# Kernel optimization log

Measured on AMD Instinct MI355X. Metric: run time of the kernel, lower is better.

The kernel has to match this reference:

```python
import jax, jax.numpy as jnp
import numpy as np

N_NODES = 65536
N_PER = 1024      # nodes per graph
NUM_GRAPHS = 64
N_EDGES = 1048576
IN_DIM = 192
PE_DIM = 64
HIDDEN = 256
LATENT = 128
POOL_RATIO = 0.5
K_PER = int(np.ceil(POOL_RATIO * N_PER))  # 512 kept per graph


def setup_inputs() -> dict:
    key = jax.random.key(0)
    ks = jax.random.split(key, 12)
    x_raw = jax.random.normal(ks[0], (N_NODES, IN_DIM), dtype=jnp.float32)
    sincos_pe = jax.random.normal(ks[1], (N_NODES, PE_DIM), dtype=jnp.float32)
    edge_index = jax.random.randint(ks[2], (2, N_EDGES), 0, N_NODES, dtype=jnp.int64)
    batch = (jnp.arange(N_NODES, dtype=jnp.int64) // N_PER)
    eps = jax.random.normal(ks[3], (N_NODES, LATENT), dtype=jnp.float32)
    # learned parameters (GCNConv: Linear no-bias weight + separate bias; TopKPooling weight)
    def glorot(k, shape):
        lim = float(np.sqrt(6.0 / (shape[0] + shape[1])))
        return jax.random.uniform(k, shape, jnp.float32, -lim, lim)
    W1 = glorot(ks[4], (IN_DIM + PE_DIM, HIDDEN))
    b1 = jnp.zeros((HIDDEN,), jnp.float32)
    Wmu = glorot(ks[5], (HIDDEN, LATENT))
    bmu = jnp.zeros((LATENT,), jnp.float32)
    Wlv = glorot(ks[6], (HIDDEN, LATENT))
    blv = jnp.zeros((LATENT,), jnp.float32)
    w_pool = jax.random.uniform(ks[7], (LATENT,), jnp.float32, -1.0, 1.0) / np.sqrt(LATENT)
    return {"x_raw": x_raw, "sincos_pe": sincos_pe, "edge_index": edge_index,
            "batch": batch, "eps": eps, "W1": W1, "b1": b1, "Wmu": Wmu,
            "bmu": bmu, "Wlv": Wlv, "blv": blv, "w_pool": w_pool}


def _gcn_conv(x, W, b, src, dst, n):
    # PyG GCNConv: x' = D^{-1/2}(A+I)D^{-1/2} (x W) + b, self-loops already in src/dst
    h = x @ W                                   # [N, out]
    deg = jnp.zeros((n,), h.dtype).at[dst].add(1.0)
    dinv = jax.lax.rsqrt(deg)                   # deg >= 1 thanks to self-loops
    norm = dinv[src] * dinv[dst]                # [E+N]
    msg = norm[:, None] * h[src]                # gather (irregular)
    return jax.ops.segment_sum(msg, dst, num_segments=n) + b


def reference(x_raw, sincos_pe, edge_index, batch, eps, W1, b1, Wmu, bmu, Wlv, blv, w_pool):
    n = x_raw.shape[0]
    loops = jnp.arange(n, dtype=edge_index.dtype)
    src = jnp.concatenate([edge_index[0], loops])
    dst = jnp.concatenate([edge_index[1], loops])

    x_in = jnp.concatenate([x_raw, sincos_pe], axis=-1)
    h = jax.nn.relu(_gcn_conv(x_in, W1, b1, src, dst, n))
    mu = _gcn_conv(h, Wmu, bmu, src, dst, n)
    logvar = _gcn_conv(h, Wlv, blv, src, dst, n)
    z = mu + eps * jnp.exp(0.5 * logvar)

    # TopKPooling: score = tanh((z . w)/||w||); keep top ratio per graph
    score = jnp.tanh((z @ w_pool) / jnp.linalg.norm(w_pool))   # [N]
    s2 = score.reshape(NUM_GRAPHS, N_PER)
    _, idx = jax.lax.top_k(s2, K_PER)                           # descending per graph
    perm = (idx + (jnp.arange(NUM_GRAPHS) * N_PER)[:, None]).reshape(-1)
    z_pool = z[perm] * score[perm][:, None]
    mu_pool = mu[perm]
    logvar_pool = logvar[perm]
    batch_pool = batch[perm]
    return z_pool, mu_pool, logvar_pool, batch_pool, perm
```

## Files before the change

### kernel.cpp

```cpp
#include <hip/hip_runtime.h>
#include <hip/hip_fp16.h>
#include <math.h>

#define NN      65536
#define NE      1048576
#define NPER    1024
#define NGRAPH  64
#define KPER    512
#define IND     192
#define PED     64
#define HID     256
#define LAT     128

#define OFF_CNT     0u
#define OFF_ROWPTR  65536u
#define OFF_CUR     132096u
#define OFF_DINV    198656u
#define OFF_EPK     264192u
#define OFF_INVWN   2361344u
#define OFF_KEEP    2361360u
#define OFF_SCORE   2395136u
#define OFF_WT1     2460672u
#define OFF_WT2     2493440u
#define OFF_T0B     2526208u
#define OFF_HB      6720512u
#define OFF_MUB     6720512u
#define OFF_LVB     10914816u

#define OUT_MU      4194304
#define OUT_LV      8388608
#define OUT_BATCH   12582912
#define OUT_PERM    12615680

typedef __attribute__((ext_vector_type(8))) short short8;
typedef __attribute__((ext_vector_type(4))) float floatx4;

__device__ __forceinline__ unsigned short f2bf(float f) {
    unsigned int u = __float_as_uint(f);
    u += 0x7FFFu + ((u >> 16) & 1u);
    return (unsigned short)(u >> 16);
}
__device__ __forceinline__ float bf2f(unsigned short u) {
    return __uint_as_float(((unsigned int)u) << 16);
}
__device__ __forceinline__ unsigned int pack2bf(float x, float y) {
    const unsigned int ux = __float_as_uint(x) + 0x8000u;
    const unsigned int uy = __float_as_uint(y) + 0x8000u;
    return __builtin_amdgcn_perm(uy, ux, 0x07060302u);
}
__device__ __forceinline__ unsigned char f2e5(float f) {
    unsigned short u = __half_as_ushort(__float2half(f));
    u += (unsigned short)(0x7Fu + ((u >> 8) & 1u));
    return (unsigned char)(u >> 8);
}
__device__ __forceinline__ unsigned int pack4e5(float v0, float v1, float v2, float v3) {
#if __has_builtin(__builtin_amdgcn_cvt_pk_bf8_f32)
    const int t0 = __builtin_amdgcn_cvt_pk_bf8_f32(v0, v1, 0, false);
    return (unsigned int)__builtin_amdgcn_cvt_pk_bf8_f32(v2, v3, t0, true);
#else
    return (unsigned int)f2e5(v0) | ((unsigned int)f2e5(v1) << 8) |
           ((unsigned int)f2e5(v2) << 16) | ((unsigned int)f2e5(v3) << 24);
#endif
}
__device__ __forceinline__ __half2 e5lo(unsigned int u) {
    return __builtin_bit_cast(__half2, __builtin_amdgcn_perm(u, 0u, 0x05000400u));
}
__device__ __forceinline__ __half2 e5hi(unsigned int u) {
    return __builtin_bit_cast(__half2, __builtin_amdgcn_perm(u, 0u, 0x07000600u));
}

__global__ __launch_bounds__(256) void k_count(const int* __restrict__ ei, int* __restrict__ cnt) {
    const int g = blockIdx.x * 256 + threadIdx.x;
    const int4 d4 = *(const int4*)(ei + NE + g * 4);
    atomicAdd(&cnt[d4.x], 1);
    atomicAdd(&cnt[d4.y], 1);
    atomicAdd(&cnt[d4.z], 1);
    atomicAdd(&cnt[d4.w], 1);
}

__global__ __launch_bounds__(256) void k_scanA(const int* __restrict__ cnt, int* __restrict__ rp,
                                               float* __restrict__ dinv, int* __restrict__ bsum) {
    __shared__ int sh[256];
    const int t = threadIdx.x, b = blockIdx.x;
    const int i = b * 256 + t;
    const int c = cnt[i];
    sh[t] = c;
    __syncthreads();
    for (int d = 1; d < 256; d <<= 1) {
        const int v = (t >= d) ? sh[t - d] : 0;
        __syncthreads();
        sh[t] += v;
        __syncthreads();
    }
    rp[i] = sh[t] - c;
    dinv[i] = 1.0f / sqrtf((float)(c + 1));
    if (t == 255) bsum[b] = sh[t];
}

__global__ __launch_bounds__(256) void k_scanB(int* __restrict__ bsum) {
    __shared__ int sh[256];
    const int t = threadIdx.x;
    const int c = bsum[t];
    sh[t] = c;
    __syncthreads();
    for (int d = 1; d < 256; d <<= 1) {
        const int v = (t >= d) ? sh[t - d] : 0;
        __syncthreads();
        sh[t] += v;
        __syncthreads();
    }
    bsum[t] = sh[t] - c;
}

__global__ __launch_bounds__(256) void k_scanC(int* __restrict__ rp, const int* __restrict__ bsum) {
    const int t = threadIdx.x, b = blockIdx.x;
    const int i = b * 256 + t;
    rp[i] += bsum[b];
    if (i == NN - 1) rp[NN] = NE;
}

__global__ __launch_bounds__(256) void k_scatter(const int* __restrict__ ei, const int* __restrict__ rp,
                                                 int* __restrict__ cur, const float* __restrict__ dinv,
                                                 int2* __restrict__ epk) {
    int e = blockIdx.x * 256 + threadIdx.x;
    int s = ei[e];
    int d = ei[NE + e];
    int pos = rp[d] + atomicAdd(&cur[d], 1);
    epk[pos] = make_int2(s, __float_as_int(dinv[s] * dinv[d]));
}

__global__ __launch_bounds__(128) void k_wnorm(const float* __restrict__ wp, float* __restrict__ invwn) {
    __shared__ float red[128];
    int t = threadIdx.x;
    float v = wp[t];
    red[t] = v * v;
    __syncthreads();
    for (int s = 64; s > 0; s >>= 1) {
        if (t < s) red[t] += red[t + s];
        __syncthreads();
    }
    if (t == 0) invwn[0] = 1.0f / sqrtf(red[0]);
}

__global__ __launch_bounds__(256) void k_prepw(const float* __restrict__ W1, const float* __restrict__ Wmu,
                                               const float* __restrict__ Wlv, unsigned short* __restrict__ wt1,
                                               unsigned short* __restrict__ wt2) {
    const int n = blockIdx.x, k = threadIdx.x;
    wt1[n * 256 + k] = f2bf(W1[k * 256 + n]);
    wt2[n * 256 + k] = f2bf((n < 128) ? Wmu[k * 128 + n] : Wlv[k * 128 + (n - 128)]);
}

template <int MODE>
__global__ __launch_bounds__(256, 2) void k_gemm(const float* __restrict__ A0f, const float* __restrict__ A1f,
                                                 const unsigned short* __restrict__ Ah,
                                                 const unsigned short* __restrict__ Wt,
                                                 unsigned char* __restrict__ Cb) {
    __shared__ unsigned short lds[2][12288];
    const int tid = threadIdx.x;
    const int w = __builtin_amdgcn_readfirstlane(tid >> 6);
    const int lane = tid & 63;
    const int l = lane & 15, q = lane >> 4;
    const int Rbase = blockIdx.x * 128;
    const int mtb = (w >> 1) * 4;
    const int ntb = (w & 1) * 8;

    const int rs = tid >> 1;
    const int ch = tid & 1;
    const int stile = rs >> 4, sl = rs & 15, q0 = ch * 2;
    const int uA = (stile * 4 + q0) * 16 + sl;

    floatx4 acc[8][4];
#pragma unroll
    for (int j = 0; j < 8; ++j)
#pragma unroll
        for (int m = 0; m < 4; ++m) acc[j][m] = (floatx4)0.0f;

    auto stage = [&](int ks, int buf) {
        if (MODE == 0) {
            const float* p; int ld, col;
            const int k = ks * 32 + ch * 16;
            if (ks < 6) { p = A0f; ld = IND; col = k; }
            else        { p = A1f; ld = PED; col = k - IND; }
            const float* src = p + (size_t)(Rbase + rs) * ld + col;
            unsigned int pk[8];
#pragma unroll
            for (int j = 0; j < 16; j += 4) {
                const float4 t = *(const float4*)(src + j);
                pk[j / 2]     = pack2bf(t.x, t.y);
                pk[j / 2 + 1] = pack2bf(t.z, t.w);
            }
            *(uint4*)&lds[buf][uA * 8]        = *(uint4*)&pk[0];
            *(uint4*)&lds[buf][(uA + 16) * 8] = *(uint4*)&pk[4];
        } else {
            const unsigned short* src = Ah + (size_t)(Rbase + rs) * 256 + ks * 32 + ch * 16;
            *(uint4*)&lds[buf][uA * 8]        = ((const uint4*)src)[0];
            *(uint4*)&lds[buf][(uA + 16) * 8] = ((const uint4*)src)[1];
        }
#pragma unroll
        for (int rep = 0; rep < 2; ++rep) {
            const int n = rep * 128 + rs;
            const unsigned short* srcB = Wt + (size_t)n * 256 + ks * 32 + ch * 16;
            const uint4 w0 = ((const uint4*)srcB)[0];
            const uint4 w1 = ((const uint4*)srcB)[1];
            const int uB = ((n >> 4) * 4 + q0) * 16 + (n & 15);
            *(uint4*)&lds[buf][4096 + uB * 8]        = w0;
            *(uint4*)&lds[buf][4096 + (uB + 16) * 8] = w1;
        }
    };

    stage(0, 0);
    __syncthreads();
#pragma unroll
    for (int ks = 0; ks < 8; ++ks) {
        const int cur = ks & 1;
        if (ks < 7) stage(ks + 1, cur ^ 1);
        short8 a[4];
#pragma unroll
        for (int m = 0; m < 4; ++m)
            a[m] = *(const short8*)&lds[cur][(((mtb + m) * 4 + q) * 16 + l) * 8];
#pragma unroll
        for (int j = 0; j < 8; ++j) {
            const short8 b = *(const short8*)&lds[cur][4096 + (((ntb + j) * 4 + q) * 16 + l) * 8];
#pragma unroll
            for (int m = 0; m < 4; ++m)
                acc[j][m] = __builtin_amdgcn_mfma_f32_16x16x32_bf16(b, a[m], acc[j][m], 0, 0, 0);
        }
        if (ks < 7) __syncthreads();
    }

#pragma unroll
    for (int m = 0; m < 4; ++m) {
        unsigned char* rbase = Cb + (size_t)(Rbase + (mtb + m) * 16 + l) * 256 + q * 4;
#pragma unroll
        for (int j = 0; j < 8; ++j) {
            const floatx4 v = acc[j][m];
            *(unsigned int*)(rbase + (ntb + j) * 16) = pack4e5(v[0], v[1], v[2], v[3]);
        }
    }
}

template <int PHASE>
__global__ __launch_bounds__(256) void k_agg(const unsigned char* __restrict__ tb, const int* __restrict__ rp,
                                             const int2* __restrict__ epk, const float* __restrict__ dinv,
                                             const float* __restrict__ bias0, const float* __restrict__ bias1,
                                             const float* __restrict__ eps, const float* __restrict__ wp,
                                             const float* __restrict__ invwn, unsigned short* __restrict__ hb,
                                             unsigned short* __restrict__ mub, unsigned short* __restrict__ lvb,
                                             float* __restrict__ score) {
    const int wv = __builtin_amdgcn_readfirstlane(threadIdx.x >> 6);
    const int lane = threadIdx.x & 63;
    const int node = blockIdx.x * 4 + wv;
    const int c0 = lane * 4;
    const float di = dinv[node];
    const unsigned char* tbc = tb + c0;

    const unsigned int vs = *(const unsigned int*)(tbc + ((size_t)node << 8));
    const __half2 ws2 = __float2half2_rn(di * di);
    __half2 a01 = __hmul2(ws2, e5lo(vs));
    __half2 a23 = __hmul2(ws2, e5hi(vs));
    __half2 b01 = __float2half2_rn(0.0f);
    __half2 b23 = __float2half2_rn(0.0f);

    const int lane8 = lane & 7;
    const int beg = rp[node], end = rp[node + 1];
    int p = beg;
    if (p + 8 <= end) {
        int2 emv = epk[p + lane8];
        int2 env = epk[p + 8 + lane8];
        unsigned int v[8];
#pragma unroll
        for (int i = 0; i < 8; ++i)
            v[i] = *(const unsigned int*)(tbc + ((size_t)__builtin_amdgcn_readlane(emv.x, i) << 8));
        while (p + 16 <= end) {
            const int2 efv = epk[p + 16 + lane8];
            unsigned int u[8];
#pragma unroll
            for (int i = 0; i < 8; ++i)
                u[i] = *(const unsigned int*)(tbc + ((size_t)__builtin_amdgcn_readlane(env.x, i) << 8));
#pragma unroll
            for (int i = 0; i < 8; i += 2) {
                const __half2 wA = __float2half2_rn(__int_as_float(__builtin_amdgcn_readlane(emv.y, i)));
                const __half2 wB = __float2half2_rn(__int_as_float(__builtin_amdgcn_readlane(emv.y, i + 1)));
                a01 = __hfma2(wA, e5lo(v[i]), a01);     a23 = __hfma2(wA, e5hi(v[i]), a23);
                b01 = __hfma2(wB, e5lo(v[i + 1]), b01); b23 = __hfma2(wB, e5hi(v[i + 1]), b23);
            }
            emv = env; env = efv;
#pragma unroll
            for (int i = 0; i < 8; ++i) v[i] = u[i];
            p += 8;
        }
#pragma unroll
        for (int i = 0; i < 8; i += 2) {
            const __half2 wA = __float2half2_rn(__int_as_float(__builtin_amdgcn_readlane(emv.y, i)));
            const __half2 wB = __float2half2_rn(__int_as_float(__builtin_amdgcn_readlane(emv.y, i + 1)));
            a01 = __hfma2(wA, e5lo(v[i]), a01);     a23 = __hfma2(wA, e5hi(v[i]), a23);
            b01 = __hfma2(wB, e5lo(v[i + 1]), b01); b23 = __hfma2(wB, e5hi(v[i + 1]), b23);
        }
        p += 8;
    }
    if (p + 4 <= end) {
        const int2 e0 = epk[p], e1 = epk[p + 1], e2 = epk[p + 2], e3 = epk[p + 3];
        const unsigned int v0 = *(const unsigned int*)(tbc + ((size_t)__builtin_amdgcn_readfirstlane(e0.x) << 8));
        const unsigned int v1 = *(const unsigned int*)(tbc + ((size_t)__builtin_amdgcn_readfirstlane(e1.x) << 8));
        const unsigned int v2 = *(const unsigned int*)(tbc + ((size_t)__builtin_amdgcn_readfirstlane(e2.x) << 8));
        const unsigned int v3 = *(const unsigned int*)(tbc + ((size_t)__builtin_amdgcn_readfirstlane(e3.x) << 8));
        const __half2 w0 = __float2half2_rn(__int_as_float(e0.y));
        const __half2 w1 = __float2half2_rn(__int_as_float(e1.y));
        const __half2 w2 = __float2half2_rn(__int_as_float(e2.y));
        const __half2 w3 = __float2half2_rn(__int_as_float(e3.y));
        a01 = __hfma2(w0, e5lo(v0), a01); a23 = __hfma2(w0, e5hi(v0), a23);
        b01 = __hfma2(w1, e5lo(v1), b01); b23 = __hfma2(w1, e5hi(v1), b23);
        a01 = __hfma2(w2, e5lo(v2), a01); a23 = __hfma2(w2, e5hi(v2), a23);
        b01 = __hfma2(w3, e5lo(v3), b01); b23 = __hfma2(w3, e5hi(v3), b23);
        p += 4;
    }
    for (; p < end; ++p) {
        const int2 e = epk[p];
        const unsigned int v = *(const unsigned int*)(tbc + ((size_t)__builtin_amdgcn_readfirstlane(e.x) << 8));
        const __half2 w2 = __float2half2_rn(__int_as_float(e.y));
        a01 = __hfma2(w2, e5lo(v), a01);
        a23 = __hfma2(w2, e5hi(v), a23);
    }
    a01 = __hadd2(a01, b01);
    a23 = __hadd2(a23, b23);
    const float2 flo = __half22float2(a01);
    const float2 fhi = __half22float2(a23);
    float4 acc = make_float4(flo.x, flo.y, fhi.x, fhi.y);

    if (PHASE == 0) {
        const float4 bb = *(const float4*)(bias0 + c0);
        ushort4 r;
        r.x = f2bf(fmaxf(acc.x + bb.x, 0.0f));
        r.y = f2bf(fmaxf(acc.y + bb.y, 0.0f));
        r.z = f2bf(fmaxf(acc.z + bb.z, 0.0f));
        r.w = f2bf(fmaxf(acc.w + bb.w, 0.0f));
        *(ushort4*)(hb + ((size_t)node << 8) + c0) = r;
    } else {
        const int cb = (lane & 31) * 4;
        const float* bias = (lane < 32) ? bias0 : bias1;
        const float4 bb = *(const float4*)(bias + cb);
        acc.x += bb.x; acc.y += bb.y; acc.z += bb.z; acc.w += bb.w;
        unsigned short* dst = (lane < 32) ? mub : lvb;
        ushort4 st;
        st.x = f2bf(acc.x); st.y = f2bf(acc.y); st.z = f2bf(acc.z); st.w = f2bf(acc.w);
        *(ushort4*)(dst + (size_t)node * 128 + cb) = st;
        float4 l4;
        l4.x = __shfl(acc.x, lane | 32, 64);
        l4.y = __shfl(acc.y, lane | 32, 64);
        l4.z = __shfl(acc.z, lane | 32, 64);
        l4.w = __shfl(acc.w, lane | 32, 64);
        float partial = 0.0f;
        if (lane < 32) {
            const float4 e4 = *(const float4*)(eps + (size_t)node * 128 + cb);
            const float4 w4 = *(const float4*)(wp + cb);
            float zx = fmaf(e4.x, expf(0.5f * l4.x), acc.x);
            float zy = fmaf(e4.y, expf(0.5f * l4.y), acc.y);
            float zz = fmaf(e4.z, expf(0.5f * l4.z), acc.z);
            float zw = fmaf(e4.w, expf(0.5f * l4.w), acc.w);
            partial = zx * w4.x + zy * w4.y + zz * w4.z + zw * w4.w;
        }
        for (int off = 16; off > 0; off >>= 1) partial += __shfl_xor(partial, off, 64);
        if (lane == 0) score[node] = tanhf(partial * invwn[0]);
    }
}

__global__ __launch_bounds__(512) void k_topk(const float* __restrict__ score, const int* __restrict__ batch,
                                              int* __restrict__ keep, float* __restrict__ out) {
    __shared__ float sk[1024];
    __shared__ int si[1024];
    const int g = blockIdx.x, t = threadIdx.x;
    for (int i = t; i < 1024; i += 512) {
        sk[i] = score[g * 1024 + i];
        si[i] = i;
    }
    __syncthreads();
    for (int k = 2; k <= 1024; k <<= 1) {
        for (int j = k >> 1; j > 0; j >>= 1) {
            for (int base = 0; base < 1024; base += 512) {
                int i = base + t;
                int ixj = i ^ j;
                if (ixj > i) {
                    float a = sk[i], b = sk[ixj];
                    int ia = si[i], ib = si[ixj];
                    bool before = (a > b) || (a == b && ia < ib);
                    bool up = ((i & k) == 0);
                    bool sw = up ? (!before) : before;
                    if (sw) {
                        sk[i] = b; si[i] = ib;
                        sk[ixj] = a; si[ixj] = ia;
                    }
                }
            }
            __syncthreads();
        }
    }
    if (t < KPER) {
        int node = g * 1024 + si[t];
        keep[g * KPER + t] = node;
        out[OUT_BATCH + g * KPER + t] = (float)batch[node];
        out[OUT_PERM + g * KPER + t] = (float)node;
    }
}

__global__ __launch_bounds__(128) void k_gather(const int* __restrict__ keep,
                                                const unsigned short* __restrict__ mub,
                                                const unsigned short* __restrict__ lvb,
                                                const float* __restrict__ eps,
                                                const float* __restrict__ score, float* __restrict__ out) {
    const int kidx = blockIdx.x;
    const int c = threadIdx.x;
    const int node = keep[kidx];
    const float m = bf2f(mub[(size_t)node * 128 + c]);
    const float l = bf2f(lvb[(size_t)node * 128 + c]);
    const float e = eps[(size_t)node * 128 + c];
    const float z = fmaf(e, expf(0.5f * l), m);
    const float s = score[node];
    out[(size_t)kidx * 128 + c] = z * s;
    out[OUT_MU + (size_t)kidx * 128 + c] = m;
    out[OUT_LV + (size_t)kidx * 128 + c] = l;
}

extern "C" void kernel_launch(void* const* d_in, const int* in_sizes, int n_in,
                              void* d_out, int out_size, void* d_ws, size_t ws_size,
                              hipStream_t stream) {
    (void)in_sizes; (void)n_in; (void)out_size; (void)ws_size;
    const float* x_raw = (const float*)d_in[0];
    const float* pe    = (const float*)d_in[1];
    const int*   ei    = (const int*)d_in[2];
    const int*   batch = (const int*)d_in[3];
    const float* eps   = (const float*)d_in[4];
    const float* W1    = (const float*)d_in[5];
    const float* b1    = (const float*)d_in[6];
    const float* Wmu   = (const float*)d_in[7];
    const float* bmu   = (const float*)d_in[8];
    const float* Wlv   = (const float*)d_in[9];
    const float* blv   = (const float*)d_in[10];
    const float* wp    = (const float*)d_in[11];
    float* ws = (float*)d_ws;
    int*  iws = (int*)d_ws;
    int2* epk = (int2*)(iws + OFF_EPK);
    unsigned short* wt1  = (unsigned short*)(ws + OFF_WT1);
    unsigned short* wt2  = (unsigned short*)(ws + OFF_WT2);
    unsigned char*  t0b  = (unsigned char*)(ws + OFF_T0B);
    unsigned short* hb16 = (unsigned short*)(ws + OFF_HB);
    unsigned short* mub  = (unsigned short*)(ws + OFF_MUB);
    unsigned short* lvb  = (unsigned short*)(ws + OFF_LVB);
    float* out = (float*)d_out;

    hipMemsetAsync(iws + OFF_CNT, 0, 65536 * 4, stream);
    hipMemsetAsync(iws + OFF_CUR, 0, 65536 * 4, stream);

    k_count<<<NE / 1024, 256, 0, stream>>>(ei, iws + OFF_CNT);
    k_scanA<<<256, 256, 0, stream>>>(iws + OFF_CNT, iws + OFF_ROWPTR, ws + OFF_DINV, iws + OFF_KEEP);
    k_scanB<<<1, 256, 0, stream>>>(iws + OFF_KEEP);
    k_scanC<<<256, 256, 0, stream>>>(iws + OFF_ROWPTR, iws + OFF_KEEP);
    k_scatter<<<NE / 256, 256, 0, stream>>>(ei, iws + OFF_ROWPTR, iws + OFF_CUR, ws + OFF_DINV, epk);
    k_wnorm<<<1, 128, 0, stream>>>(wp, ws + OFF_INVWN);
    k_prepw<<<256, 256, 0, stream>>>(W1, Wmu, Wlv, wt1, wt2);

    k_gemm<0><<<NN / 128, 256, 0, stream>>>(x_raw, pe, nullptr, wt1, t0b);
    k_agg<0><<<NN / 4, 256, 0, stream>>>(t0b, iws + OFF_ROWPTR, epk, ws + OFF_DINV,
                                         b1, nullptr, nullptr, nullptr, nullptr,
                                         hb16, nullptr, nullptr, nullptr);
    k_gemm<1><<<NN / 128, 256, 0, stream>>>(nullptr, nullptr, hb16, wt2, t0b);
    k_agg<1><<<NN / 4, 256, 0, stream>>>(t0b, iws + OFF_ROWPTR, epk, ws + OFF_DINV,
                                         bmu, blv, eps, wp, ws + OFF_INVWN,
                                         nullptr, mub, lvb, ws + OFF_SCORE);
    k_topk<<<NGRAPH, 512, 0, stream>>>(ws + OFF_SCORE, batch, iws + OFF_KEEP, out);
    k_gather<<<NGRAPH * KPER, 128, 0, stream>>>(iws + OFF_KEEP, mub, lvb, eps,
                                                ws + OFF_SCORE, out);
}
```

Baseline: 422.3 us.

## Slice fp8 feature table by column, pack edge metadata, atomically accumulate score

The GEMM output is stored column-sliced (32-byte slices per node), so each aggregation wave handles 8 nodes by 32 columns and gathers hit a smaller, cache-friendlier slice. Edge records are packed into 32 bits (16-bit source index plus fp16 weight), halving the edge stream. The score is now built from partial sums via atomicAdd across slices, with tanh moved into the gather kernel. Because per-lane work now runs serially over each node's edges with a per-lane data-dependent loop, wave divergence and the extra atomics may cost time. The 16-bit source index is enough only because there are 65536 nodes.

```diff
diff --git a/kernel.cpp b/kernel.cpp
--- a/kernel.cpp
+++ b/kernel.cpp
@@ -68,6 +68,9 @@
 __device__ __forceinline__ __half2 e5hi(unsigned int u) {
     return __builtin_bit_cast(__half2, __builtin_amdgcn_perm(u, 0u, 0x07000600u));
 }
+__device__ __forceinline__ __half2 meta2w(unsigned int m) {
+    return __builtin_bit_cast(__half2, __builtin_amdgcn_perm(m, m, 0x07060706u));
+}
 
 __global__ __launch_bounds__(256) void k_count(const int* __restrict__ ei, int* __restrict__ cnt) {
     const int g = blockIdx.x * 256 + threadIdx.x;
@@ -121,12 +124,13 @@
 
 __global__ __launch_bounds__(256) void k_scatter(const int* __restrict__ ei, const int* __restrict__ rp,
                                                  int* __restrict__ cur, const float* __restrict__ dinv,
-                                                 int2* __restrict__ epk) {
+                                                 unsigned int* __restrict__ epk) {
     int e = blockIdx.x * 256 + threadIdx.x;
     int s = ei[e];
     int d = ei[NE + e];
     int pos = rp[d] + atomicAdd(&cur[d], 1);
-    epk[pos] = make_int2(s, __float_as_int(dinv[s] * dinv[d]));
+    const unsigned short hn = __half_as_ushort(__float2half(dinv[s] * dinv[d]));
+    epk[pos] = ((unsigned int)hn << 16) | (unsigned int)s;
 }
 
 __global__ __launch_bounds__(128) void k_wnorm(const float* __restrict__ wp, float* __restrict__ invwn) {
@@ -230,137 +234,99 @@
 
 #pragma unroll
     for (int m = 0; m < 4; ++m) {
-        unsigned char* rbase = Cb + (size_t)(Rbase + (mtb + m) * 16 + l) * 256 + q * 4;
+        const int row = Rbase + (mtb + m) * 16 + l;
 #pragma unroll
         for (int j = 0; j < 8; ++j) {
+            const int col = (ntb + j) * 16 + q * 4;
             const floatx4 v = acc[j][m];
-            *(unsigned int*)(rbase + (ntb + j) * 16) = pack4e5(v[0], v[1], v[2], v[3]);
+            *(unsigned int*)(Cb + ((size_t)(col >> 5) * NN + row) * 32 + (col & 31)) =
+                pack4e5(v[0], v[1], v[2], v[3]);
         }
     }
 }
 
 template <int PHASE>
 __global__ __launch_bounds__(256) void k_agg(const unsigned char* __restrict__ tb, const int* __restrict__ rp,
-                                             const int2* __restrict__ epk, const float* __restrict__ dinv,
+                                             const unsigned int* __restrict__ epk, const float* __restrict__ dinv,
                                              const float* __restrict__ bias0, const float* __restrict__ bias1,
                                              const float* __restrict__ eps, const float* __restrict__ wp,
-                                             const float* __restrict__ invwn, unsigned short* __restrict__ hb,
-                                             unsigned short* __restrict__ mub, unsigned short* __restrict__ lvb,
-                                             float* __restrict__ score) {
-    const int wv = __builtin_amdgcn_readfirstlane(threadIdx.x >> 6);
+                                             unsigned short* __restrict__ hb, unsigned short* __restrict__ mub,
+                                             unsigned short* __restrict__ lvb, float* __restrict__ score) {
     const int lane = threadIdx.x & 63;
-    const int node = blockIdx.x * 4 + wv;
-    const int c0 = lane * 4;
+    const int slice = blockIdx.x & 7;
+    const int node = (blockIdx.x >> 3) * 32 + (threadIdx.x >> 6) * 8 + (lane >> 3);
+    const int lo4 = (lane & 7) * 4;
+    const unsigned char* tsl = tb + ((size_t)slice * NN) * 32 + lo4;
+
     const float di = dinv[node];
-    const unsigned char* tbc = tb + c0;
-
-    const unsigned int vs = *(const unsigned int*)(tbc + ((size_t)node << 8));
+    const unsigned int vs = *(const unsigned int*)(tsl + ((size_t)node << 5));
     const __half2 ws2 = __float2half2_rn(di * di);
     __half2 a01 = __hmul2(ws2, e5lo(vs));
     __half2 a23 = __hmul2(ws2, e5hi(vs));
     __half2 b01 = __float2half2_rn(0.0f);
     __half2 b23 = __float2half2_rn(0.0f);
 
-    const int lane8 = lane & 7;
-    const int beg = rp[node], end = rp[node + 1];
-    int p = beg;
-    if (p + 8 <= end) {
-        int2 emv = epk[p + lane8];
-        int2 env = epk[p + 8 + lane8];
-        unsigned int v[8];
-#pragma unroll
-        for (int i = 0; i < 8; ++i)
-            v[i] = *(const unsigned int*)(tbc + ((size_t)__builtin_amdgcn_readlane(emv.x, i) << 8));
-        while (p + 16 <= end) {
-            const int2 efv = epk[p + 16 + lane8];
-            unsigned int u[8];
-#pragma unroll
-            for (int i = 0; i < 8; ++i)
-                u[i] = *(const unsigned int*)(tbc + ((size_t)__builtin_amdgcn_readlane(env.x, i) << 8));
-#pragma unroll
-            for (int i = 0; i < 8; i += 2) {
-                const __half2 wA = __float2half2_rn(__int_as_float(__builtin_amdgcn_readlane(emv.y, i)));
-                const __half2 wB = __float2half2_rn(__int_as_float(__builtin_amdgcn_readlane(emv.y, i + 1)));
-                a01 = __hfma2(wA, e5lo(v[i]), a01);     a23 = __hfma2(wA, e5hi(v[i]), a23);
-                b01 = __hfma2(wB, e5lo(v[i + 1]), b01); b23 = __hfma2(wB, e5hi(v[i + 1]), b23);
-            }
-            emv = env; env = efv;
-#pragma unroll
-            for (int i = 0; i < 8; ++i) v[i] = u[i];
-            p += 8;
-        }
-#pragma unroll
-        for (int i = 0; i < 8; i += 2) {
-            const __half2 wA = __float2half2_rn(__int_as_float(__builtin_amdgcn_readlane(emv.y, i)));
-            const __half2 wB = __float2half2_rn(__int_as_float(__builtin_amdgcn_readlane(emv.y, i + 1)));
-            a01 = __hfma2(wA, e5lo(v[i]), a01);     a23 = __hfma2(wA, e5hi(v[i]), a23);
-            b01 = __hfma2(wB, e5lo(v[i + 1]), b01); b23 = __hfma2(wB, e5hi(v[i + 1]), b23);
-        }
-        p += 8;
-    }
-    if (p + 4 <= end) {
-        const int2 e0 = epk[p], e1 = epk[p + 1], e2 = epk[p + 2], e3 = epk[p + 3];
-        const unsigned int v0 = *(const unsigned int*)(tbc + ((size_t)__builtin_amdgcn_readfirstlane(e0.x) << 8));
-        const unsigned int v1 = *(const unsigned int*)(tbc + ((size_t)__builtin_amdgcn_readfirstlane(e1.x) << 8));
-        const unsigned int v2 = *(const unsigned int*)(tbc + ((size_t)__builtin_amdgcn_readfirstlane(e2.x) << 8));
-        const unsigned int v3 = *(const unsigned int*)(tbc + ((size_t)__builtin_amdgcn_readfirstlane(e3.x) << 8));
-        const __half2 w0 = __float2half2_rn(__int_as_float(e0.y));
-        const __half2 w1 = __float2half2_rn(__int_as_float(e1.y));
-        const __half2 w2 = __float2half2_rn(__int_as_float(e2.y));
-        const __half2 w3 = __float2half2_rn(__int_as_float(e3.y));
+    int p = rp[node];
+    const int end = rp[node + 1];
+    unsigned int m0 = epk[p], m1 = epk[p + 1];
+    unsigned int v0 = *(const unsigned int*)(tsl + ((size_t)(m0 & 0xFFFFu) << 5));
+    unsigned int v1 = *(const unsigned int*)(tsl + ((size_t)(m1 & 0xFFFFu) << 5));
+    while (p + 2 <= end) {
+        const unsigned int n0 = epk[p + 2], n1 = epk[p + 3];
+        const unsigned int u0 = *(const unsigned int*)(tsl + ((size_t)(n0 & 0xFFFFu) << 5));
+        const unsigned int u1 = *(const unsigned int*)(tsl + ((size_t)(n1 & 0xFFFFu) << 5));
+        const __half2 w0 = meta2w(m0);
+        const __half2 w1 = meta2w(m1);
         a01 = __hfma2(w0, e5lo(v0), a01); a23 = __hfma2(w0, e5hi(v0), a23);
         b01 = __hfma2(w1, e5lo(v1), b01); b23 = __hfma2(w1, e5hi(v1), b23);
-        a01 = __hfma2(w2, e5lo(v2), a01); a23 = __hfma2(w2, e5hi(v2), a23);
-        b01 = __hfma2(w3, e5lo(v3), b01); b23 = __hfma2(w3, e5hi(v3), b23);
-        p += 4;
-    }
-    for (; p < end; ++p) {
-        const int2 e = epk[p];
-        const unsigned int v = *(const unsigned int*)(tbc + ((size_t)__builtin_amdgcn_readfirstlane(e.x) << 8));
-        const __half2 w2 = __float2half2_rn(__int_as_float(e.y));
-        a01 = __hfma2(w2, e5lo(v), a01);
-        a23 = __hfma2(w2, e5hi(v), a23);
+        m0 = n0; m1 = n1; v0 = u0; v1 = u1; p += 2;
+    }
+    if (p < end) {
+        const __half2 w0 = meta2w(m0);
+        a01 = __hfma2(w0, e5lo(v0), a01);
+        a23 = __hfma2(w0, e5hi(v0), a23);
     }
     a01 = __hadd2(a01, b01);
     a23 = __hadd2(a23, b23);
     const float2 flo = __half22float2(a01);
     const float2 fhi = __half22float2(a23);
     float4 acc = make_float4(flo.x, flo.y, fhi.x, fhi.y);
+    const int c = slice * 32 + lo4;
 
     if (PHASE == 0) {
-        const float4 bb = *(const float4*)(bias0 + c0);
+        const float4 bb = *(const float4*)(bias0 + c);
         ushort4 r;
         r.x = f2bf(fmaxf(acc.x + bb.x, 0.0f));
         r.y = f2bf(fmaxf(acc.y + bb.y, 0.0f));
         r.z = f2bf(fmaxf(acc.z + bb.z, 0.0f));
         r.w = f2bf(fmaxf(acc.w + bb.w, 0.0f));
-        *(ushort4*)(hb + ((size_t)node << 8) + c0) = r;
+        *(ushort4*)(hb + (size_t)node * 256 + c) = r;
     } else {
-        const int cb = (lane & 31) * 4;
-        const float* bias = (lane < 32) ? bias0 : bias1;
-        const float4 bb = *(const float4*)(bias + cb);
-        acc.x += bb.x; acc.y += bb.y; acc.z += bb.z; acc.w += bb.w;
-        unsigned short* dst = (lane < 32) ? mub : lvb;
-        ushort4 st;
-        st.x = f2bf(acc.x); st.y = f2bf(acc.y); st.z = f2bf(acc.z); st.w = f2bf(acc.w);
-        *(ushort4*)(dst + (size_t)node * 128 + cb) = st;
-        float4 l4;
-        l4.x = __shfl(acc.x, lane | 32, 64);
-        l4.y = __shfl(acc.y, lane | 32, 64);
-        l4.z = __shfl(acc.z, lane | 32, 64);
-        l4.w = __shfl(acc.w, lane | 32, 64);
-        float partial = 0.0f;
-        if (lane < 32) {
-            const float4 e4 = *(const float4*)(eps + (size_t)node * 128 + cb);
-            const float4 w4 = *(const float4*)(wp + cb);
-            float zx = fmaf(e4.x, expf(0.5f * l4.x), acc.x);
-            float zy = fmaf(e4.y, expf(0.5f * l4.y), acc.y);
-            float zz = fmaf(e4.z, expf(0.5f * l4.z), acc.z);
-            float zw = fmaf(e4.w, expf(0.5f * l4.w), acc.w);
-            partial = zx * w4.x + zy * w4.y + zz * w4.z + zw * w4.w;
-        }
-        for (int off = 16; off > 0; off >>= 1) partial += __shfl_xor(partial, off, 64);
-        if (lane == 0) score[node] = tanhf(partial * invwn[0]);
+        float partial;
+        if (c < 128) {
+            const float4 bb = *(const float4*)(bias0 + c);
+            acc.x += bb.x; acc.y += bb.y; acc.z += bb.z; acc.w += bb.w;
+            ushort4 st;
+            st.x = f2bf(acc.x); st.y = f2bf(acc.y); st.z = f2bf(acc.z); st.w = f2bf(acc.w);
+            *(ushort4*)(mub + (size_t)node * 128 + c) = st;
+            const float4 w4 = *(const float4*)(wp + c);
+            partial = acc.x * w4.x + acc.y * w4.y + acc.z * w4.z + acc.w * w4.w;
+        } else {
+            const int cl = c - 128;
+            const float4 bb = *(const float4*)(bias1 + cl);
+            acc.x += bb.x; acc.y += bb.y; acc.z += bb.z; acc.w += bb.w;
+            ushort4 st;
+            st.x = f2bf(acc.x); st.y = f2bf(acc.y); st.z = f2bf(acc.z); st.w = f2bf(acc.w);
+            *(ushort4*)(lvb + (size_t)node * 128 + cl) = st;
+            const float4 w4 = *(const float4*)(wp + cl);
+            const float4 e4 = *(const float4*)(eps + (size_t)node * 128 + cl);
+            partial = e4.x * expf(0.5f * acc.x) * w4.x + e4.y * expf(0.5f * acc.y) * w4.y +
+                      e4.z * expf(0.5f * acc.z) * w4.z + e4.w * expf(0.5f * acc.w) * w4.w;
+        }
+        partial += __shfl_xor(partial, 1, 64);
+        partial += __shfl_xor(partial, 2, 64);
+        partial += __shfl_xor(partial, 4, 64);
+        if ((lane & 7) == 0) atomicAdd(&score[node], partial);
     }
 }
 
@@ -406,7 +372,8 @@
                                                 const unsigned short* __restrict__ mub,
                                                 const unsigned short* __restrict__ lvb,
                                                 const float* __restrict__ eps,
-                                                const float* __restrict__ score, float* __restrict__ out) {
+                                                const float* __restrict__ score,
+                                                const float* __restrict__ invwn, float* __restrict__ out) {
     const int kidx = blockIdx.x;
     const int c = threadIdx.x;
     const int node = keep[kidx];
@@ -414,7 +381,7 @@
     const float l = bf2f(lvb[(size_t)node * 128 + c]);
     const float e = eps[(size_t)node * 128 + c];
     const float z = fmaf(e, expf(0.5f * l), m);
-    const float s = score[node];
+    const float s = tanhf(score[node] * invwn[0]);
     out[(size_t)kidx * 128 + c] = z * s;
     out[OUT_MU + (size_t)kidx * 128 + c] = m;
     out[OUT_LV + (size_t)kidx * 128 + c] = l;
@@ -438,7 +405,7 @@
     const float* wp    = (const float*)d_in[11];
     float* ws = (float*)d_ws;
     int*  iws = (int*)d_ws;
-    int2* epk = (int2*)(iws + OFF_EPK);
+    unsigned int* epk = (unsigned int*)(iws + OFF_EPK);
     unsigned short* wt1  = (unsigned short*)(ws + OFF_WT1);
     unsigned short* wt2  = (unsigned short*)(ws + OFF_WT2);
     unsigned char*  t0b  = (unsigned char*)(ws + OFF_T0B);
@@ -449,6 +416,7 @@
 
     hipMemsetAsync(iws + OFF_CNT, 0, 65536 * 4, stream);
     hipMemsetAsync(iws + OFF_CUR, 0, 65536 * 4, stream);
+    hipMemsetAsync(ws + OFF_SCORE, 0, 65536 * 4, stream);
 
     k_count<<<NE / 1024, 256, 0, stream>>>(ei, iws + OFF_CNT);
     k_scanA<<<256, 256, 0, stream>>>(iws + OFF_CNT, iws + OFF_ROWPTR, ws + OFF_DINV, iws + OFF_KEEP);
@@ -459,14 +427,14 @@
     k_prepw<<<256, 256, 0, stream>>>(W1, Wmu, Wlv, wt1, wt2);
 
     k_gemm<0><<<NN / 128, 256, 0, stream>>>(x_raw, pe, nullptr, wt1, t0b);
-    k_agg<0><<<NN / 4, 256, 0, stream>>>(t0b, iws + OFF_ROWPTR, epk, ws + OFF_DINV,
-                                         b1, nullptr, nullptr, nullptr, nullptr,
-                                         hb16, nullptr, nullptr, nullptr);
+    k_agg<0><<<(NN / 32) * 8, 256, 0, stream>>>(t0b, iws + OFF_ROWPTR, epk, ws + OFF_DINV,
+                                                b1, nullptr, nullptr, nullptr,
+                                                hb16, nullptr, nullptr, nullptr);
     k_gemm<1><<<NN / 128, 256, 0, stream>>>(nullptr, nullptr, hb16, wt2, t0b);
-    k_agg<1><<<NN / 4, 256, 0, stream>>>(t0b, iws + OFF_ROWPTR, epk, ws + OFF_DINV,
-                                         bmu, blv, eps, wp, ws + OFF_INVWN,
-                                         nullptr, mub, lvb, ws + OFF_SCORE);
+    k_agg<1><<<(NN / 32) * 8, 256, 0, stream>>>(t0b, iws + OFF_ROWPTR, epk, ws + OFF_DINV,
+                                                bmu, blv, eps, wp,
+                                                nullptr, mub, lvb, ws + OFF_SCORE);
     k_topk<<<NGRAPH, 512, 0, stream>>>(ws + OFF_SCORE, batch, iws + OFF_KEEP, out);
     k_gather<<<NGRAPH * KPER, 128, 0, stream>>>(iws + OFF_KEEP, mub, lvb, eps,
-                                                ws + OFF_SCORE, out);
-}
+                                                ws + OFF_SCORE, ws + OFF_INVWN, out);
+}
```

New measurement: 493.5 us. 1.17x slower.
